# Optimization experiments

Measured on AMD Instinct MI355X. Metric: run time of the kernel, lower is better.

The kernel has to match this reference:

```python
import jax, jax.numpy as jnp
import numpy as np

D = 1024; H = 8; QLR = 384; KVLR = 256; NOPE = 128; ROPE = 64; VD = 128
E = 8; TOPK = 2; INTER = 512; NSH = 2; B = 2; T = 2048
QKD = NOPE + ROPE  # 192


def _rms(x, w, eps=1e-6):
    return x * jax.lax.rsqrt(jnp.mean(x * x, axis=-1, keepdims=True) + eps) * w


def _rope(x, cos, sin):
    # x: [B,T,h,ROPE]; pairs are consecutive elements (torch view(...,-1,2)).
    x0 = x[..., 0::2]
    x1 = x[..., 1::2]
    c = cos[None, :, None, :]
    s = sin[None, :, None, :]
    y0 = x0 * c - x1 * s
    y1 = x0 * s + x1 * c
    return jnp.stack([y0, y1], axis=-1).reshape(x.shape)


def setup_inputs() -> dict:
    key = jax.random.key(0)
    ks = jax.random.split(key, 12)
    def w(k, shape, scale=0.02):
        return jax.random.normal(k, shape, dtype=jnp.float32) * scale
    inv = 1.0 / (10000.0 ** (jnp.arange(0, ROPE, 2, dtype=jnp.float32) / ROPE))
    ang = jnp.arange(T, dtype=jnp.float32)[:, None] * inv[None, :]  # [T, ROPE//2]
    return {
        "x": jax.random.normal(ks[0], (B, T, D), dtype=jnp.float32),
        "freqs_cos": jnp.cos(ang),
        "freqs_sin": jnp.sin(ang),
        "rmsn1_w": jnp.ones((D,), jnp.float32),
        "rmsn2_w": jnp.ones((D,), jnp.float32),
        "latent_w": w(ks[1], (D, QLR + KVLR + ROPE)),
        "q_norm_w": jnp.ones((QLR,), jnp.float32),
        "q_up_w": w(ks[2], (QLR, H * QKD)),
        "kv_norm_w": jnp.ones((KVLR,), jnp.float32),
        "kv_up_w": w(ks[3], (KVLR, H * (NOPE + VD))),
        "c_proj_w": w(ks[4], (D, D)),
        "gate_w": w(ks[5], (D, E)),
        "sh_w1": w(ks[6], (D, INTER * NSH)),
        "sh_w2": w(ks[7], (INTER * NSH, D)),
        "sh_w3": w(ks[8], (D, INTER * NSH)),
        "e_w1": w(ks[9], (E, D, INTER)),
        "e_w2": w(ks[10], (E, INTER, D)),
        "e_w3": w(ks[11], (E, D, INTER)),
    }


def reference(x, freqs_cos, freqs_sin, rmsn1_w, rmsn2_w, latent_w, q_norm_w,
              q_up_w, kv_norm_w, kv_up_w, c_proj_w, gate_w, sh_w1, sh_w2,
              sh_w3, e_w1, e_w2, e_w3):
    Bx, Tx, _ = x.shape
    # ---- MLA attention ----
    h = _rms(x, rmsn1_w)
    lat = h @ latent_w
    q_l, kv_l, k_r = jnp.split(lat, [QLR, QLR + KVLR], axis=-1)
    q = (_rms(q_l, q_norm_w) @ q_up_w).reshape(Bx, Tx, H, QKD)
    q_n, q_r = q[..., :NOPE], q[..., NOPE:]
    q_r = _rope(q_r, freqs_cos, freqs_sin)
    q = jnp.concatenate([q_n, q_r], axis=-1)  # [B,T,H,QKD]
    kv = (_rms(kv_l, kv_norm_w) @ kv_up_w).reshape(Bx, Tx, H, NOPE + VD)
    k_n, v = kv[..., :NOPE], kv[..., NOPE:]
    k_r = _rope(k_r[:, :, None, :], freqs_cos, freqs_sin)
    k_r = jnp.broadcast_to(k_r, (Bx, Tx, H, ROPE))
    k = jnp.concatenate([k_n, k_r], axis=-1)
    scale = 1.0 / jnp.sqrt(jnp.float32(QKD))
    scores = jnp.einsum('bqhd,bkhd->bhqk', q, k) * scale
    causal = jnp.tril(jnp.ones((Tx, Tx), dtype=bool))
    scores = jnp.where(causal, scores, jnp.finfo(scores.dtype).min)
    attn = jax.nn.softmax(scores, axis=-1)
    y = jnp.einsum('bhqk,bkhd->bqhd', attn, v).reshape(Bx, Tx, D)
    x = x + y @ c_proj_w
    # ---- DeepSeekMoE ----
    h2 = _rms(x, rmsn2_w).reshape(-1, D)  # [N, D]
    y_sh = (jax.nn.silu(h2 @ sh_w1) * (h2 @ sh_w3)) @ sh_w2
    scores_g = jax.nn.softmax(h2 @ gate_w, axis=-1)  # [N, E]
    w_top, idx = jax.lax.top_k(scores_g, TOPK)  # weights == gathered original scores
    # combine weights per expert (route_scale = 1.0)
    cw = jnp.sum(jax.nn.one_hot(idx, E, dtype=h2.dtype) * w_top[..., None], axis=1)  # [N, E]
    h1 = jnp.einsum('nd,edi->eni', h2, e_w1)
    h3 = jnp.einsum('nd,edi->eni', h2, e_w3)
    out_e = jnp.einsum('eni,eid->end', jax.nn.silu(h1) * h3, e_w2)  # [E, N, D]
    y_moe = y_sh + jnp.einsum('end,ne->nd', out_e, cw)
    return x + y_moe.reshape(Bx, Tx, D)
```

## Files before the change

kernel.cpp:

```cpp
#include <hip/hip_runtime.h>
#include <hip/hip_bf16.h>
#include <math.h>

#define D_ 1024
#define H_ 8
#define QLR_ 384
#define KVLR_ 256
#define NOPE_ 128
#define ROPE_ 64
#define VD_ 128
#define E_ 8
#define INTER_ 512
#define B_ 2
#define T_ 2048
#define QKD_ 192
#define NTOK (B_*T_)
#define LSTR 4608
#define MAXMB 72

typedef __attribute__((ext_vector_type(8))) short short8;
typedef __attribute__((ext_vector_type(4))) float f32x4;
typedef __attribute__((ext_vector_type(4))) unsigned short us4;

__device__ __forceinline__ unsigned short f2bf(float f) {
  union { float f; unsigned u; } v; v.f = f;
  return (unsigned short)((v.u + 0x7FFFu + ((v.u >> 16) & 1u)) >> 16);
}
__device__ __forceinline__ float bf2f(unsigned short h) {
  union { unsigned u; float f; } v; v.u = ((unsigned)h) << 16;
  return v.f;
}

#define GLD16(SRC, DST) __builtin_amdgcn_global_load_lds( \
    (__attribute__((address_space(1))) void*)(SRC), \
    (__attribute__((address_space(3))) void*)(DST), 16, 0, 0)

#define DPPF(v, ctrl) __int_as_float(__builtin_amdgcn_update_dpp(0, __float_as_int(v), ctrl, 0xF, 0xF, true))
__device__ __forceinline__ float dppmax16(float v) {
  v = fmaxf(v, DPPF(v, 0xB1));
  v = fmaxf(v, DPPF(v, 0x4E));
  v = fmaxf(v, DPPF(v, 0x124));
  v = fmaxf(v, DPPF(v, 0x128));
  return v;
}
__device__ __forceinline__ float dppsum16(float v) {
  v += DPPF(v, 0xB1);
  v += DPPF(v, 0x4E);
  v += DPPF(v, 0x124);
  v += DPPF(v, 0x128);
  return v;
}

__device__ __forceinline__ void trans32(const float* __restrict__ src, unsigned short* __restrict__ dst,
                                        int R, int C, int c0, int r0, float (*tile)[33]) {
  int tx = threadIdx.x & 31, ty = threadIdx.x >> 5;
  #pragma unroll
  for (int i = 0; i < 4; ++i) {
    int rr = ty + i * 8;
    tile[rr][tx] = src[(size_t)(r0 + rr) * C + c0 + tx];
  }
  __syncthreads();
  #pragma unroll
  for (int i = 0; i < 4; ++i) {
    int rr = ty + i * 8;
    dst[(size_t)(c0 + rr) * R + r0 + tx] = f2bf(tile[tx][rr]);
  }
}
__device__ __forceinline__ void trans32p(const float* __restrict__ src, unsigned short* __restrict__ dst,
                                         int K, int C1, int c0, int r0, int f, float (*tile)[33]) {
  int tx = threadIdx.x & 31, ty = threadIdx.x >> 5;
  #pragma unroll
  for (int i = 0; i < 4; ++i) {
    int rr = ty + i * 8;
    tile[rr][tx] = src[(size_t)(r0 + rr) * C1 + c0 + tx];
  }
  __syncthreads();
  #pragma unroll
  for (int i = 0; i < 4; ++i) {
    int cc = ty + i * 8;
    int c = c0 + cc;
    int n = ((c >> 4) << 5) + (c & 15) + f;
    dst[(size_t)n * K + r0 + tx] = f2bf(tile[tx][cc]);
  }
}

__global__ __launch_bounds__(256) void prep1(
    const float* __restrict__ x, const float* __restrict__ rw, unsigned short* __restrict__ h_bf,
    const float* __restrict__ latent_w, unsigned short* __restrict__ Wlat) {
  __shared__ float tile[32][33];
  int b = blockIdx.x;
  if (b < NTOK) {
    int tid = threadIdx.x;
    const float* xr = x + (size_t)b * D_;
    float v[4]; float ss = 0.f;
    #pragma unroll
    for (int j = 0; j < 4; ++j) { v[j] = xr[tid + j * 256]; ss += v[j] * v[j]; }
    for (int o = 1; o < 64; o <<= 1) ss += __shfl_xor(ss, o);
    if ((tid & 63) == 0) tile[32][tid >> 6] = ss;
    __syncthreads();
    float inv = 1.f / sqrtf((tile[32][0] + tile[32][1] + tile[32][2] + tile[32][3]) / D_ + 1e-6f);
    #pragma unroll
    for (int j = 0; j < 4; ++j) {
      int i = tid + j * 256;
      h_bf[(size_t)b * D_ + i] = f2bf(v[j] * inv * rw[i]);
    }
    return;
  }
  b -= NTOK;
  trans32(latent_w, Wlat, 1024, 704, (b % 22) * 32, (b / 22) * 32, tile);
}

__global__ __launch_bounds__(256) void prep2(
    const unsigned short* __restrict__ h_bf, const unsigned short* __restrict__ Wlat,
    unsigned short* __restrict__ lat,
    const float* __restrict__ q_up_w, unsigned short* __restrict__ Wqup,
    const float* __restrict__ kv_up_w, unsigned short* __restrict__ Wkv,
    const float* __restrict__ c_proj_w, unsigned short* __restrict__ Wcp,
    const float* __restrict__ sh_w1, const float* __restrict__ sh_w3, unsigned short* __restrict__ Wsh13,
    const float* __restrict__ sh_w2, unsigned short* __restrict__ Wsh2,
    const float* __restrict__ e_w1, const float* __restrict__ e_w3, unsigned short* __restrict__ Wew13,
    const float* __restrict__ e_w2, unsigned short* __restrict__ Wew2) {
  __shared__ __align__(16) unsigned short As[128 * 32];
  __shared__ __align__(16) unsigned short Bs[128 * 32];
  __shared__ float tile[32][33];
  int b = blockIdx.x;
  if (b < 192) {
    const int tid = threadIdx.x, lane = tid & 63, wave = tid >> 6;
    const int wm = wave >> 1, wn = wave & 1;
    const int bm = (b / 6) * 128, bn = (b % 6) * 128;
    const int r = lane & 15, g = lane >> 4;
    f32x4 acc[4][4];
    #pragma unroll
    for (int i = 0; i < 4; ++i)
      #pragma unroll
      for (int j = 0; j < 4; ++j) acc[i][j] = (f32x4)0.f;
    const int rl0 = wave * 16 + (lane >> 2), rl1 = rl0 + 64;
    const int kc = (lane & 3) * 8;
    char* AsB = (char*)As; char* BsB = (char*)Bs;
    for (int k0 = 0; k0 < 1024; k0 += 32) {
      GLD16(h_bf + (size_t)(bm + rl0) * 1024 + k0 + kc, AsB + wave * 1024);
      GLD16(h_bf + (size_t)(bm + rl1) * 1024 + k0 + kc, AsB + (wave + 4) * 1024);
      GLD16(Wlat + (size_t)(bn + rl0) * 1024 + k0 + kc, BsB + wave * 1024);
      GLD16(Wlat + (size_t)(bn + rl1) * 1024 + k0 + kc, BsB + (wave + 4) * 1024);
      __syncthreads();
      short8 af[4], bfr[4];
      #pragma unroll
      for (int mi = 0; mi < 4; ++mi)
        af[mi] = *(const short8*)(As + (wm * 64 + mi * 16 + r) * 32 + g * 8);
      #pragma unroll
      for (int nj = 0; nj < 4; ++nj)
        bfr[nj] = *(const short8*)(Bs + (wn * 64 + nj * 16 + r) * 32 + g * 8);
      #pragma unroll
      for (int mi = 0; mi < 4; ++mi)
        #pragma unroll
        for (int nj = 0; nj < 4; ++nj)
          acc[mi][nj] = __builtin_amdgcn_mfma_f32_16x16x32_bf16(af[mi], bfr[nj], acc[mi][nj], 0, 0, 0);
      __syncthreads();
    }
    const int orow0 = wm * 64 + g * 4;
    const int ocol0 = bn + wn * 64 + r;
    #pragma unroll
    for (int mi = 0; mi < 4; ++mi)
      #pragma unroll
      for (int reg = 0; reg < 4; ++reg) {
        int mrow = bm + orow0 + mi * 16 + reg;
        size_t bas = (size_t)mrow * 768 + ocol0;
        #pragma unroll
        for (int nj = 0; nj < 4; ++nj) lat[bas + nj * 16] = f2bf(acc[mi][nj][reg]);
      }
    return;
  }
  b -= 192;
  if (b < 576) { trans32(q_up_w, Wqup, 384, 1536, (b % 48) * 32, (b / 48) * 32, tile); return; }
  b -= 576;
  if (b < 512) { trans32(kv_up_w, Wkv, 256, 2048, (b % 64) * 32, (b / 64) * 32, tile); return; }
  b -= 512;
  if (b < 1024) { trans32(c_proj_w, Wcp, 1024, 1024, (b % 32) * 32, (b / 32) * 32, tile); return; }
  b -= 1024;
  if (b < 1024) { trans32(sh_w2, Wsh2, 1024, 1024, (b % 32) * 32, (b / 32) * 32, tile); return; }
  b -= 1024;
  if (b < 2048) {
    int z = b / 1024, idx = b % 1024;
    trans32p(z ? sh_w3 : sh_w1, Wsh13, 1024, 1024, (idx % 32) * 32, (idx / 32) * 32, z * 16, tile);
    return;
  }
  b -= 2048;
  if (b < 8192) {
    int z = b / 512, idx = b % 512;
    int bat = z >> 1, f = (z & 1) * 16;
    const float* src = ((z & 1) ? e_w3 : e_w1) + (size_t)bat * 1024 * 512;
    trans32p(src, Wew13 + (size_t)bat * 1024 * 1024, 1024, 512, (idx % 16) * 32, (idx / 16) * 32, f, tile);
    return;
  }
  b -= 8192;
  {
    int z = b / 512, idx = b % 512;
    trans32(e_w2 + (size_t)z * 512 * 1024, Wew2 + (size_t)z * 1024 * 512,
            512, 1024, (idx % 32) * 32, (idx / 32) * 32, tile);
  }
}

__global__ __launch_bounds__(256) void lat_post(
    const unsigned short* __restrict__ lat, const float* __restrict__ qw,
    const float* __restrict__ kw, const float* __restrict__ fc, const float* __restrict__ fs,
    unsigned short* __restrict__ qn, unsigned short* __restrict__ kvn,
    unsigned short* __restrict__ kr) {
  int row = blockIdx.x, tid = threadIdx.x;
  int lane = tid & 63, wv = tid >> 6;
  const unsigned short* lr = lat + (size_t)row * 768;
  float s1 = 0.f, s2 = 0.f;
  for (int i = tid; i < QLR_; i += 256) { float v = bf2f(lr[i]); s1 += v * v; }
  { float v = bf2f(lr[QLR_ + tid]); s2 = v * v; }
  for (int o = 1; o < 64; o <<= 1) { s1 += __shfl_xor(s1, o); s2 += __shfl_xor(s2, o); }
  __shared__ float red[8];
  if (lane == 0) { red[wv] = s1; red[4 + wv] = s2; }
  __syncthreads();
  float inv1 = 1.f / sqrtf((red[0] + red[1] + red[2] + red[3]) / QLR_ + 1e-6f);
  float inv2 = 1.f / sqrtf((red[4] + red[5] + red[6] + red[7]) / KVLR_ + 1e-6f);
  for (int i = tid; i < QLR_; i += 256)
    qn[(size_t)row * QLR_ + i] = f2bf(bf2f(lr[i]) * inv1 * qw[i]);
  kvn[(size_t)row * KVLR_ + tid] = f2bf(bf2f(lr[QLR_ + tid]) * inv2 * kw[tid]);
  if (tid < 32) {
    int t = row & (T_ - 1);
    float c = fc[t * 32 + tid], s = fs[t * 32 + tid];
    float x0 = bf2f(lr[640 + 2 * tid]), x1 = bf2f(lr[640 + 2 * tid + 1]);
    kr[(size_t)row * ROPE_ + 2 * tid]     = f2bf(x0 * c - x1 * s);
    kr[(size_t)row * ROPE_ + 2 * tid + 1] = f2bf(x0 * s + x1 * c);
  }
}

template<int MODE>
__global__ __launch_bounds__(256) void gemm_bf16(
    const unsigned short* __restrict__ A, const unsigned short* __restrict__ Bt,
    void* __restrict__ Cv, int M, int N, int K,
    const float* __restrict__ addv) {
  __shared__ __align__(16) unsigned short As[128 * 32];
  __shared__ __align__(16) unsigned short Bs[128 * 32];
  const int tid = threadIdx.x;
  const int lane = tid & 63, wave = tid >> 6;
  const int wm = wave >> 1, wn = wave & 1;
  const int bm = blockIdx.y * 128, bn = blockIdx.x * 128;
  const int r = lane & 15, g = lane >> 4;

  f32x4 acc[4][4];
  #pragma unroll
  for (int i = 0; i < 4; ++i)
    #pragma unroll
    for (int j = 0; j < 4; ++j) acc[i][j] = (f32x4)0.f;

  const int rl0 = wave * 16 + (lane >> 2);
  const int rl1 = rl0 + 64;
  const int kc = (lane & 3) * 8;
  char* AsB = (char*)As; char* BsB = (char*)Bs;

  for (int k0 = 0; k0 < K; k0 += 32) {
    GLD16(A + (size_t)(bm + rl0) * K + k0 + kc, AsB + wave * 1024);
    GLD16(A + (size_t)(bm + rl1) * K + k0 + kc, AsB + (wave + 4) * 1024);
    GLD16(Bt + (size_t)(bn + rl0) * K + k0 + kc, BsB + wave * 1024);
    GLD16(Bt + (size_t)(bn + rl1) * K + k0 + kc, BsB + (wave + 4) * 1024);
    __syncthreads();
    short8 af[4], bfr[4];
    #pragma unroll
    for (int mi = 0; mi < 4; ++mi)
      af[mi] = *(const short8*)(As + (wm * 64 + mi * 16 + r) * 32 + g * 8);
    #pragma unroll
    for (int nj = 0; nj < 4; ++nj)
      bfr[nj] = *(const short8*)(Bs + (wn * 64 + nj * 16 + r) * 32 + g * 8);
    #pragma unroll
    for (int mi = 0; mi < 4; ++mi)
      #pragma unroll
      for (int nj = 0; nj < 4; ++nj)
        acc[mi][nj] = __builtin_amdgcn_mfma_f32_16x16x32_bf16(af[mi], bfr[nj], acc[mi][nj], 0, 0, 0);
    __syncthreads();
  }

  const int orow0 = wm * 64 + g * 4;
  const int ocol0 = bn + wn * 64 + r;
  #pragma unroll
  for (int mi = 0; mi < 4; ++mi) {
    #pragma unroll
    for (int reg = 0; reg < 4; ++reg) {
      int mrow = bm + orow0 + mi * 16 + reg;
      size_t bas = (size_t)mrow * N + ocol0;
      if (MODE == 0) {
        unsigned short* C = (unsigned short*)Cv;
        #pragma unroll
        for (int nj = 0; nj < 4; ++nj) C[bas + nj * 16] = f2bf(acc[mi][nj][reg]);
      } else {
        float* C = (float*)Cv;
        #pragma unroll
        for (int nj = 0; nj < 4; ++nj) C[bas + nj * 16] = acc[mi][nj][reg] + addv[bas + nj * 16];
      }
    }
  }
}

__global__ __launch_bounds__(256) void gemm_qkv(
    const unsigned short* __restrict__ qn, const unsigned short* __restrict__ Wqup,
    const unsigned short* __restrict__ kvn, const unsigned short* __restrict__ Wkv,
    unsigned short* __restrict__ qq, unsigned short* __restrict__ kvb,
    unsigned short* __restrict__ vtg) {
  __shared__ __align__(16) unsigned short As[128 * 32];
  __shared__ __align__(16) unsigned short Bs[128 * 32];
  const int tid = threadIdx.x;
  const int lane = tid & 63, wave = tid >> 6;
  const int wm = wave >> 1, wn = wave & 1;
  const bool isQ = blockIdx.x < 12;
  const int bx = isQ ? blockIdx.x : blockIdx.x - 12;
  const unsigned short* A  = isQ ? qn : kvn;
  const unsigned short* Bt = isQ ? Wqup : Wkv;
  const int K = isQ ? QLR_ : KVLR_;
  const int bm = blockIdx.y * 128, bn = bx * 128;
  const int r = lane & 15, g = lane >> 4;

  f32x4 acc[4][4];
  #pragma unroll
  for (int i = 0; i < 4; ++i)
    #pragma unroll
    for (int j = 0; j < 4; ++j) acc[i][j] = (f32x4)0.f;

  const int rl0 = wave * 16 + (lane >> 2);
  const int rl1 = rl0 + 64;
  const int kc = (lane & 3) * 8;
  char* AsB = (char*)As; char* BsB = (char*)Bs;

  for (int k0 = 0; k0 < K; k0 += 32) {
    GLD16(A + (size_t)(bm + rl0) * K + k0 + kc, AsB + wave * 1024);
    GLD16(A + (size_t)(bm + rl1) * K + k0 + kc, AsB + (wave + 4) * 1024);
    GLD16(Bt + (size_t)(bn + rl0) * K + k0 + kc, BsB + wave * 1024);
    GLD16(Bt + (size_t)(bn + rl1) * K + k0 + kc, BsB + (wave + 4) * 1024);
    __syncthreads();
    short8 af[4], bfr[4];
    #pragma unroll
    for (int mi = 0; mi < 4; ++mi)
      af[mi] = *(const short8*)(As + (wm * 64 + mi * 16 + r) * 32 + g * 8);
    #pragma unroll
    for (int nj = 0; nj < 4; ++nj)
      bfr[nj] = *(const short8*)(Bs + (wn * 64 + nj * 16 + r) * 32 + g * 8);
    #pragma unroll
    for (int mi = 0; mi < 4; ++mi)
      #pragma unroll
      for (int nj = 0; nj < 4; ++nj)
        acc[mi][nj] = __builtin_amdgcn_mfma_f32_16x16x32_bf16(af[mi], bfr[nj], acc[mi][nj], 0, 0, 0);
    __syncthreads();
  }

  if (isQ) {
    const int orow0 = wm * 64 + g * 4;
    const int ocol0 = bn + wn * 64 + r;
    #pragma unroll
    for (int mi = 0; mi < 4; ++mi)
      #pragma unroll
      for (int reg = 0; reg < 4; ++reg) {
        int mrow = bm + orow0 + mi * 16 + reg;
        size_t bas = (size_t)mrow * 1536 + ocol0;
        #pragma unroll
        for (int nj = 0; nj < 4; ++nj) qq[bas + nj * 16] = f2bf(acc[mi][nj][reg]);
      }
  } else {
    const int colbase = bn + wn * 64;
    const int b = bm >> 11;
    const int hh = colbase >> 8;
    if ((colbase & 255) < 128) {
      #pragma unroll
      for (int mi = 0; mi < 4; ++mi)
        #pragma unroll
        for (int reg = 0; reg < 4; ++reg) {
          int mrow = bm + wm * 64 + mi * 16 + g * 4 + reg;
          size_t bas = (size_t)mrow * 1024 + hh * 128 + (colbase & 255) + r;
          #pragma unroll
          for (int nj = 0; nj < 4; ++nj) kvb[bas + nj * 16] = f2bf(acc[mi][nj][reg]);
        }
    } else {
      const int tl0 = (bm & 2047) + wm * 64 + g * 4;
      const int d0 = (colbase & 255) - 128 + r;
      const size_t bhbase = (size_t)(b * 8 + hh) * 64;
      #pragma unroll
      for (int mi = 0; mi < 4; ++mi) {
        int t = tl0 + mi * 16;
        size_t tb = (bhbase + (t >> 5)) * 4096 + (t & 31);
        #pragma unroll
        for (int nj = 0; nj < 4; ++nj) {
          int d = d0 + nj * 16;
          us4 pk;
          #pragma unroll
          for (int reg = 0; reg < 4; ++reg) pk[reg] = f2bf(acc[mi][nj][reg]);
          *(us4*)(vtg + tb + (size_t)d * 32) = pk;
        }
      }
    }
  }
}

__global__ __launch_bounds__(256) void gemm_ffn13(
    const unsigned short* __restrict__ h2b, const unsigned short* __restrict__ Wsh13,
    unsigned short* __restrict__ t1m,
    const unsigned short* __restrict__ Wew13, unsigned short* __restrict__ ehm,
    const int* __restrict__ lists, const int* __restrict__ map, const int* __restrict__ sbase) {
  __shared__ __align__(16) unsigned short As[128 * 32];
  __shared__ __align__(16) unsigned short Bs[128 * 32];
  const int i = blockIdx.x;
  const bool isSh = i < 512;
  const int tid = threadIdx.x, lane = tid & 63, wave = tid >> 6;
  const int wm = wave >> 1, wn = wave & 1;
  const int r = lane & 15, g = lane >> 4;
  const int rl0 = wave * 16 + (lane >> 2), rl1 = rl0 + 64;
  const int kc = (lane & 3) * 8;

  int bn, e = 0, ib = 0, bm = 0;
  const unsigned short* Bt;
  int ar0, ar1;
  const unsigned short* A;
  if (isSh) {
    bn = (i & 15) * 128; bm = (i >> 4) * 128;
    Bt = Wsh13; A = h2b;
    ar0 = bm + rl0; ar1 = bm + rl1;
  } else {
    int j = i - 512;
    bn = (j & 7) * 128;
    int mb = map[j >> 3];
    if (mb < 0) return;
    e = mb >> 16; ib = mb & 0xFFFF;
    Bt = Wew13 + (size_t)e * 1024 * 1024; A = h2b;
    ar0 = lists[e * LSTR + ib * 128 + rl0]; if (ar0 < 0) ar0 = 0;
    ar1 = lists[e * LSTR + ib * 128 + rl1]; if (ar1 < 0) ar1 = 0;
  }

  f32x4 acc[4][4];
  #pragma unroll
  for (int a = 0; a < 4; ++a)
    #pragma unroll
    for (int bj = 0; bj < 4; ++bj) acc[a][bj] = (f32x4)0.f;
  char* AsB = (char*)As; char* BsB = (char*)Bs;

  for (int k0 = 0; k0 < 1024; k0 += 32) {
    GLD16(A + (size_t)ar0 * 1024 + k0 + kc, AsB + wave * 1024);
    GLD16(A + (size_t)ar1 * 1024 + k0 + kc, AsB + (wave + 4) * 1024);
    GLD16(Bt + (size_t)(bn + rl0) * 1024 + k0 + kc, BsB + wave * 1024);
    GLD16(Bt + (size_t)(bn + rl1) * 1024 + k0 + kc, BsB + (wave + 4) * 1024);
    __syncthreads();
    short8 af[4], bfr[4];
    #pragma unroll
    for (int mi = 0; mi < 4; ++mi)
      af[mi] = *(const short8*)(As + (wm * 64 + mi * 16 + r) * 32 + g * 8);
    #pragma unroll
    for (int nj = 0; nj < 4; ++nj)
      bfr[nj] = *(const short8*)(Bs + (wn * 64 + nj * 16 + r) * 32 + g * 8);
    #pragma unroll
    for (int mi = 0; mi < 4; ++mi)
      #pragma unroll
      for (int nj = 0; nj < 4; ++nj)
        acc[mi][nj] = __builtin_amdgcn_mfma_f32_16x16x32_bf16(af[mi], bfr[nj], acc[mi][nj], 0, 0, 0);
    __syncthreads();
  }

  if (isSh) {
    const int hc = ((bn + wn * 64) >> 1) + r;
    #pragma unroll
    for (int mi = 0; mi < 4; ++mi)
      #pragma unroll
      for (int reg = 0; reg < 4; ++reg) {
        int mrow = bm + wm * 64 + mi * 16 + g * 4 + reg;
        #pragma unroll
        for (int p = 0; p < 2; ++p) {
          float a = acc[mi][2 * p][reg], b3 = acc[mi][2 * p + 1][reg];
          t1m[(size_t)mrow * 1024 + hc + p * 16] = f2bf((a / (1.f + __expf(-a))) * b3);
        }
      }
  } else {
    const int sb = sbase[e] + ib * 128;
    const int hc = ((bn + wn * 64) >> 1) + r;
    #pragma unroll
    for (int mi = 0; mi < 4; ++mi)
      #pragma unroll
      for (int reg = 0; reg < 4; ++reg) {
        int srow = sb + wm * 64 + mi * 16 + g * 4 + reg;
        #pragma unroll
        for (int p = 0; p < 2; ++p) {
          float a = acc[mi][2 * p][reg], b3 = acc[mi][2 * p + 1][reg];
          ehm[(size_t)srow * 512 + hc + p * 16] = f2bf((a / (1.f + __expf(-a))) * b3);
        }
      }
  }
}

__global__ __launch_bounds__(256) void gemm_ffn2(
    const unsigned short* __restrict__ t1m, const unsigned short* __restrict__ Wsh2,
    const unsigned short* __restrict__ ehm, const unsigned short* __restrict__ Wew2,
    float* __restrict__ out,
    const int* __restrict__ lists, const int* __restrict__ map, const int* __restrict__ sbase,
    const float* __restrict__ cw) {
  __shared__ __align__(16) unsigned short As[128 * 32];
  __shared__ __align__(16) unsigned short Bs[128 * 32];
  const int i = blockIdx.x;
  const bool isSh = i < 256;
  const int tid = threadIdx.x, lane = tid & 63, wave = tid >> 6;
  const int wm = wave >> 1, wn = wave & 1;
  const int r = lane & 15, g = lane >> 4;
  const int rl0 = wave * 16 + (lane >> 2), rl1 = rl0 + 64;
  const int kc = (lane & 3) * 8;

  int bn, e = 0, ib = 0, bm = 0, K;
  const unsigned short* A;
  const unsigned short* Bt;
  if (isSh) {
    bn = (i & 7) * 128; bm = (i >> 3) * 128;
    A = t1m; Bt = Wsh2; K = 1024;
  } else {
    int j = i - 256;
    bn = (j & 7) * 128;
    int mb = map[j >> 3];
    if (mb < 0) return;
    e = mb >> 16; ib = mb & 0xFFFF;
    bm = sbase[e] + ib * 128;
    A = ehm; Bt = Wew2 + (size_t)e * 512 * 1024; K = 512;
  }

  f32x4 acc[4][4];
  #pragma unroll
  for (int a = 0; a < 4; ++a)
    #pragma unroll
    for (int bj = 0; bj < 4; ++bj) acc[a][bj] = (f32x4)0.f;
  char* AsB = (char*)As; char* BsB = (char*)Bs;

  for (int k0 = 0; k0 < K; k0 += 32) {
    GLD16(A + (size_t)(bm + rl0) * K + k0 + kc, AsB + wave * 1024);
    GLD16(A + (size_t)(bm + rl1) * K + k0 + kc, AsB + (wave + 4) * 1024);
    GLD16(Bt + (size_t)(bn + rl0) * K + k0 + kc, BsB + wave * 1024);
    GLD16(Bt + (size_t)(bn + rl1) * K + k0 + kc, BsB + (wave + 4) * 1024);
    __syncthreads();
    short8 af[4], bfr[4];
    #pragma unroll
    for (int mi = 0; mi < 4; ++mi)
      af[mi] = *(const short8*)(As + (wm * 64 + mi * 16 + r) * 32 + g * 8);
    #pragma unroll
    for (int nj = 0; nj < 4; ++nj)
      bfr[nj] = *(const short8*)(Bs + (wn * 64 + nj * 16 + r) * 32 + g * 8);
    #pragma unroll
    for (int mi = 0; mi < 4; ++mi)
      #pragma unroll
      for (int nj = 0; nj < 4; ++nj)
        acc[mi][nj] = __builtin_amdgcn_mfma_f32_16x16x32_bf16(af[mi], bfr[nj], acc[mi][nj], 0, 0, 0);
    __syncthreads();
  }

  const int ocol0 = bn + wn * 64 + r;
  if (isSh) {
    #pragma unroll
    for (int mi = 0; mi < 4; ++mi)
      #pragma unroll
      for (int reg = 0; reg < 4; ++reg) {
        int mrow = bm + wm * 64 + mi * 16 + g * 4 + reg;
        #pragma unroll
        for (int nj = 0; nj < 4; ++nj)
          atomicAdd(out + (size_t)mrow * 1024 + ocol0 + nj * 16, acc[mi][nj][reg]);
      }
  } else {
    #pragma unroll
    for (int mi = 0; mi < 4; ++mi)
      #pragma unroll
      for (int reg = 0; reg < 4; ++reg) {
        int orow = wm * 64 + mi * 16 + g * 4 + reg;
        int tok = lists[e * LSTR + ib * 128 + orow];
        if (tok >= 0) {
          float wt = cw[(size_t)tok * E_ + e];
          #pragma unroll
          for (int nj = 0; nj < 4; ++nj)
            atomicAdd(out + (size_t)tok * 1024 + ocol0 + nj * 16, acc[mi][nj][reg] * wt);
        }
      }
  }
}

#define AQ 128
#define AK 32
#define VP 40
__global__ __launch_bounds__(512) void attn_mfma(
    const unsigned short* __restrict__ q,
    const unsigned short* __restrict__ kv,
    const unsigned short* __restrict__ kr,
    const unsigned short* __restrict__ vt,
    const float* __restrict__ fcos, const float* __restrict__ fsin,
    unsigned short* __restrict__ po,
    float* __restrict__ pml) {
  __shared__ __align__(16) unsigned short Ks[AK * 192];
  __shared__ __align__(16) unsigned short Vl[128 * VP];
  __shared__ __align__(16) unsigned short Ps[8 * 16 * VP];
  const int tid = threadIdx.x, lane = tid & 63, wave = tid >> 6;
  const int r = lane & 15, g = lane >> 4;
  const int bh = blockIdx.y, b = bh >> 3, h = bh & 7;
  const int Stab[17] = {0,1,2,3,4,6,8,10,12,15,18,21,24,28,32,36,40};
  const int cid = 39 - (int)blockIdx.x;
  int qt = 0;
  #pragma unroll
  for (int t = 1; t <= 15; ++t) if (cid >= Stab[t]) qt = t;
  const int chunk = cid - Stab[qt];
  const int q0 = qt * AQ;
  const int ntl = 4 * (qt + 1);
  const int kb = chunk * 16;
  const int ke = (kb + 16 < ntl) ? kb + 16 : ntl;
  const size_t bT = (size_t)b * T_;
  const unsigned short* vbase = vt + (size_t)bh * 64 * 4096;
  char* KsB = (char*)Ks;

  short8 qf[6];
  const int qrow = q0 + wave * 16 + r;
  {
    const unsigned short* qb = q + ((bT + qrow) * H_ + h) * 192;
    #pragma unroll
    for (int kk = 0; kk < 6; ++kk) qf[kk] = *(const short8*)(qb + kk * 32 + g * 8);
    #pragma unroll
    for (int kk = 4; kk < 6; ++kk) {
      int i0 = (kk - 4) * 16 + g * 4;
      #pragma unroll
      for (int p = 0; p < 4; ++p) {
        float cc = fcos[qrow * 32 + i0 + p], sn = fsin[qrow * 32 + i0 + p];
        float x0 = bf2f((unsigned short)qf[kk][2 * p]), x1 = bf2f((unsigned short)qf[kk][2 * p + 1]);
        qf[kk][2 * p]     = (short)f2bf(x0 * cc - x1 * sn);
        qf[kk][2 * p + 1] = (short)f2bf(x0 * sn + x1 * cc);
      }
    }
  }

  float m_i[4], l_i[4];
  f32x4 o[8];
  #pragma unroll
  for (int i = 0; i < 4; ++i) { m_i[i] = -1e30f; l_i[i] = 0.f; }
  #pragma unroll
  for (int cb = 0; cb < 8; ++cb) o[cb] = (f32x4)0.f;

  const float scale2 = 0.07216878364870322f * 1.44269504088896f;

  const int kr0r = tid / 24, kr0c = tid % 24;
  const bool k1v = tid < 256;
  const int kr1r = (tid + 512) / 24, kr1c = (tid + 512) % 24;

  short8 kreg0, kreg1, vreg;
  {
    int kk0 = kb * AK;
    kreg0 = (kr0c < 16)
      ? *(const short8*)(kv + ((bT + kk0 + kr0r) * H_ + h) * 128 + kr0c * 8)
      : *(const short8*)(kr + (bT + kk0 + kr0r) * 64 + (kr0c - 16) * 8);
    if (k1v)
      kreg1 = (kr1c < 16)
        ? *(const short8*)(kv + ((bT + kk0 + kr1r) * H_ + h) * 128 + kr1c * 8)
        : *(const short8*)(kr + (bT + kk0 + kr1r) * 64 + (kr1c - 16) * 8);
    vreg = *(const short8*)(vbase + (size_t)kb * 4096 + tid * 8);
  }

  for (int kt = kb; kt < ke; ++kt) {
    __builtin_amdgcn_s_barrier();
    __builtin_amdgcn_sched_barrier(0);
    *(short8*)(KsB + ((kr0r * 384 + kr0c * 16) ^ ((kr0r & 7) << 4))) = kreg0;
    if (k1v)
      *(short8*)(KsB + ((kr1r * 384 + kr1c * 16) ^ ((kr1r & 7) << 4))) = kreg1;
    *(short8*)(Vl + (tid >> 2) * VP + (tid & 3) * 8) = vreg;
    asm volatile("s_waitcnt lgkmcnt(0)" ::: "memory");
    __builtin_amdgcn_s_barrier();
    __builtin_amdgcn_sched_barrier(0);

    if (kt + 1 < ke) {
      int k1 = (kt + 1) * AK;
      kreg0 = (kr0c < 16)
        ? *(const short8*)(kv + ((bT + k1 + kr0r) * H_ + h) * 128 + kr0c * 8)
        : *(const short8*)(kr + (bT + k1 + kr0r) * 64 + (kr0c - 16) * 8);
      if (k1v)
        kreg1 = (kr1c < 16)
          ? *(const short8*)(kv + ((bT + k1 + kr1r) * H_ + h) * 128 + kr1c * 8)
          : *(const short8*)(kr + (bT + k1 + kr1r) * 64 + (kr1c - 16) * 8);
      vreg = *(const short8*)(vbase + (size_t)(kt + 1) * 4096 + tid * 8);
    }

    const int k0 = kt * AK;
    f32x4 sf0 = (f32x4)0.f, sf1 = (f32x4)0.f;
    {
      int ksw = (r & 7) << 4;
      __builtin_amdgcn_s_setprio(1);
      #pragma unroll
      for (int kk = 0; kk < 6; ++kk) {
        short8 b0 = *(const short8*)(KsB + ((r * 384 + kk * 64 + g * 16) ^ ksw));
        short8 b1 = *(const short8*)(KsB + (((16 + r) * 384 + kk * 64 + g * 16) ^ ksw));
        sf0 = __builtin_amdgcn_mfma_f32_16x16x32_bf16(qf[kk], b0, sf0, 0, 0, 0);
        sf1 = __builtin_amdgcn_mfma_f32_16x16x32_bf16(qf[kk], b1, sf1, 0, 0, 0);
      }
      __builtin_amdgcn_s_setprio(0);
    }

    float fac[4];
    bool needs = false;
    const bool bnd = (k0 + AK > q0);
    #pragma unroll
    for (int reg = 0; reg < 4; ++reg) {
      float s0 = sf0[reg] * scale2;
      float s1 = sf1[reg] * scale2;
      if (bnd) {
        int qp = q0 + wave * 16 + g * 4 + reg;
        if (k0 + r > qp) s0 = -1e30f;
        if (k0 + 16 + r > qp) s1 = -1e30f;
      }
      float mt = dppmax16(fmaxf(s0, s1));
      float fc = 1.f, mn = m_i[reg];
      if (mt > mn + 8.f) {
        mn = mt; fc = exp2f(m_i[reg] - mn); m_i[reg] = mn; needs = true;
      }
      float e0 = exp2f(s0 - mn), e1 = exp2f(s1 - mn);
      float rs = dppsum16(e0 + e1);
      l_i[reg] = l_i[reg] * fc + rs;
      fac[reg] = fc;
      __hip_bfloat162 pk = __float22bfloat162_rn(float2{e0, e1});
      unsigned u = *(unsigned*)&pk;
      int prow = g * 4 + reg;
      Ps[wave * 16 * VP + prow * VP + r] = (unsigned short)u;
      Ps[wave * 16 * VP + prow * VP + 16 + r] = (unsigned short)(u >> 16);
    }
    if (__any(needs)) {
      #pragma unroll
      for (int cb = 0; cb < 8; ++cb)
        #pragma unroll
        for (int reg = 0; reg < 4; ++reg) o[cb][reg] *= fac[reg];
    }
    short8 pa = *(const short8*)(Ps + wave * 16 * VP + r * VP + g * 8);
    __builtin_amdgcn_s_setprio(1);
    #pragma unroll
    for (int cb = 0; cb < 8; ++cb) {
      short8 vb = *(const short8*)(Vl + (cb * 16 + r) * VP + g * 8);
      o[cb] = __builtin_amdgcn_mfma_f32_16x16x32_bf16(pa, vb, o[cb], 0, 0, 0);
    }
    __builtin_amdgcn_s_setprio(0);
  }

  const int slab = bh * 40 + cid;
  unsigned short* pob = po + (size_t)slab * 16384;
  float* pmlb = pml + (size_t)slab * 256;
  #pragma unroll
  for (int reg = 0; reg < 4; ++reg) {
    int row = wave * 16 + g * 4 + reg;
    if (r == 0) { pmlb[row * 2] = m_i[reg]; pmlb[row * 2 + 1] = l_i[reg]; }
    #pragma unroll
    for (int cb = 0; cb < 8; ++cb)
      pob[row * 128 + cb * 16 + r] = f2bf(o[cb][reg]);
  }
}

__global__ __launch_bounds__(512) void attn_combine(
    const unsigned short* __restrict__ po, const float* __restrict__ pml,
    unsigned short* __restrict__ y) {
  const int qt = blockIdx.x, bh = blockIdx.y, b = bh >> 3, h = bh & 7;
  const int Stab[17] = {0,1,2,3,4,6,8,10,12,15,18,21,24,28,32,36,40};
  const int s0 = bh * 40 + Stab[qt];
  const int nc = Stab[qt + 1] - Stab[qt];
  const int row = threadIdx.x >> 2;
  const int qp = threadIdx.x & 3;
  float mj[4], lj[4];
  float m = -1e30f;
  for (int j = 0; j < nc; ++j) {
    mj[j] = pml[(size_t)(s0 + j) * 256 + row * 2];
    lj[j] = pml[(size_t)(s0 + j) * 256 + row * 2 + 1];
    m = fmaxf(m, mj[j]);
  }
  float lsum = 0.f;
  float ej[4];
  for (int j = 0; j < nc; ++j) {
    ej[j] = exp2f(mj[j] - m);
    lsum += lj[j] * ej[j];
  }
  float inv = 1.f / lsum;
  unsigned short* yb = y + ((size_t)(b * T_ + qt * 128 + row)) * 1024 + h * 128 + qp * 32;
  #pragma unroll
  for (int v = 0; v < 4; ++v) {
    float accv[8];
    #pragma unroll
    for (int jj = 0; jj < 8; ++jj) accv[jj] = 0.f;
    for (int j = 0; j < nc; ++j) {
      const unsigned short* oj = po + (size_t)(s0 + j) * 16384 + row * 128 + qp * 32 + v * 8;
      short8 a = *(const short8*)oj;
      float w = ej[j];
      #pragma unroll
      for (int jj = 0; jj < 8; ++jj) accv[jj] += bf2f((unsigned short)a[jj]) * w;
    }
    short8 wv;
    #pragma unroll
    for (int jj = 0; jj < 8; ++jj) wv[jj] = (short)f2bf(accv[jj] * inv);
    *(short8*)(yb + v * 8) = wv;
  }
}

__global__ __launch_bounds__(256) void rms2_gate(
    const float* __restrict__ xo, const float* __restrict__ rw, const float* __restrict__ gw,
    unsigned short* __restrict__ h2b, float* __restrict__ cw) {
  int row = blockIdx.x, tid = threadIdx.x;
  int lane = tid & 63, wv = tid >> 6;
  const float* xr = xo + (size_t)row * D_;
  float v[4]; float ss = 0.f;
  #pragma unroll
  for (int j = 0; j < 4; ++j) { v[j] = xr[tid + j * 256]; ss += v[j] * v[j]; }
  for (int o = 1; o < 64; o <<= 1) ss += __shfl_xor(ss, o);
  __shared__ float red[4];
  if (lane == 0) red[wv] = ss;
  __syncthreads();
  float inv = 1.f / sqrtf((red[0] + red[1] + red[2] + red[3]) / D_ + 1e-6f);
  float a[E_] = {0, 0, 0, 0, 0, 0, 0, 0};
  #pragma unroll
  for (int j = 0; j < 4; ++j) {
    int i = tid + j * 256;
    float hv = v[j] * inv * rw[i];
    h2b[(size_t)row * D_ + i] = f2bf(hv);
    const float* wr = gw + (size_t)i * E_;
    #pragma unroll
    for (int e = 0; e < E_; ++e) a[e] += hv * wr[e];
  }
  #pragma unroll
  for (int e = 0; e < E_; ++e) {
    float t = a[e];
    for (int o = 1; o < 64; o <<= 1) t += __shfl_xor(t, o);
    a[e] = t;
  }
  __shared__ float ga[4][E_];
  if (lane == 0)
    #pragma unroll
    for (int e = 0; e < E_; ++e) ga[wv][e] = a[e];
  __syncthreads();
  if (tid == 0) {
    float lg[E_];
    #pragma unroll
    for (int e = 0; e < E_; ++e) lg[e] = ga[0][e] + ga[1][e] + ga[2][e] + ga[3][e];
    float mx = lg[0];
    #pragma unroll
    for (int e = 1; e < E_; ++e) mx = fmaxf(mx, lg[e]);
    float sum = 0.f; float p[E_];
    #pragma unroll
    for (int e = 0; e < E_; ++e) { p[e] = __expf(lg[e] - mx); sum += p[e]; }
    float is = 1.f / sum;
    int i1 = 0; float b1 = p[0];
    #pragma unroll
    for (int e = 1; e < E_; ++e) if (p[e] > b1) { b1 = p[e]; i1 = e; }
    int i2 = -1; float b2 = -1.f;
    #pragma unroll
    for (int e = 0; e < E_; ++e) if (e != i1 && p[e] > b2) { b2 = p[e]; i2 = e; }
    #pragma unroll
    for (int e = 0; e < E_; ++e)
      cw[(size_t)row * E_ + e] = (e == i1) ? b1 * is : (e == i2 ? b2 * is : 0.f);
  }
}

__global__ __launch_bounds__(256) void moe_build(const float* __restrict__ cw,
                                                 int* __restrict__ lists, int* __restrict__ counts) {
  int e = blockIdx.x, tid = threadIdx.x;
  int lane = tid & 63, wv = tid >> 6;
  __shared__ int wsum[4];
  __shared__ int base;
  if (tid == 0) base = 0;
  __syncthreads();
  for (int c0 = 0; c0 < NTOK; c0 += 256) {
    int tok = c0 + tid;
    bool f = cw[(size_t)tok * E_ + e] > 0.f;
    unsigned long long m = __ballot(f);
    int pos = __popcll(m & ((1ull << lane) - 1ull));
    if (lane == 0) wsum[wv] = __popcll(m);
    __syncthreads();
    int woff = base;
    #pragma unroll
    for (int w = 0; w < 4; ++w) if (w < wv) woff += wsum[w];
    if (f) lists[e * LSTR + woff + pos] = tok;
    __syncthreads();
    if (tid == 0) base += wsum[0] + wsum[1] + wsum[2] + wsum[3];
    __syncthreads();
  }
  int cnt = base;
  int padded = (cnt + 127) & ~127;
  for (int i2 = cnt + tid; i2 < padded; i2 += 256) lists[e * LSTR + i2] = -1;
  if (tid == 0) { counts[e] = cnt; counts[8 + e] = padded >> 7; }
}

__global__ void moe_finalize(const int* __restrict__ counts, int* __restrict__ map,
                             int* __restrict__ sbase) {
  if (threadIdx.x == 0 && blockIdx.x == 0) {
    int cum = 0;
    for (int e = 0; e < E_; ++e) {
      sbase[e] = cum * 128;
      int nb = counts[8 + e];
      for (int i = 0; i < nb; ++i) map[cum + i] = (e << 16) | i;
      cum += nb;
    }
    for (; cum < MAXMB; ++cum) map[cum] = -1;
  }
}

extern "C" void kernel_launch(void* const* d_in, const int* in_sizes, int n_in,
                              void* d_out, int out_size, void* d_ws, size_t ws_size,
                              hipStream_t stream) {
  const float* x        = (const float*)d_in[0];
  const float* fcos     = (const float*)d_in[1];
  const float* fsin     = (const float*)d_in[2];
  const float* rmsn1_w  = (const float*)d_in[3];
  const float* rmsn2_w  = (const float*)d_in[4];
  const float* latent_w = (const float*)d_in[5];
  const float* q_norm_w = (const float*)d_in[6];
  const float* q_up_w   = (const float*)d_in[7];
  const float* kv_norm_w= (const float*)d_in[8];
  const float* kv_up_w  = (const float*)d_in[9];
  const float* c_proj_w = (const float*)d_in[10];
  const float* gate_w   = (const float*)d_in[11];
  const float* sh_w1    = (const float*)d_in[12];
  const float* sh_w2    = (const float*)d_in[13];
  const float* sh_w3    = (const float*)d_in[14];
  const float* e_w1     = (const float*)d_in[15];
  const float* e_w2     = (const float*)d_in[16];
  const float* e_w3     = (const float*)d_in[17];
  float* out = (float*)d_out;

  char* base = (char*)d_ws;
  size_t off = 0;
  auto take = [&](size_t bytes) { char* p = base + off; off += (bytes + 255) & ~(size_t)255; return p; };
  unsigned short* Wlat  = (unsigned short*)take((size_t)768 * 1024 * 2);
  unsigned short* Wqup  = (unsigned short*)take((size_t)1536 * 384 * 2);
  unsigned short* Wkv   = (unsigned short*)take((size_t)2048 * 256 * 2);
  unsigned short* Wcp   = (unsigned short*)take((size_t)1024 * 1024 * 2);
  unsigned short* Wsh13 = (unsigned short*)take((size_t)2048 * 1024 * 2);
  unsigned short* Wsh2  = (unsigned short*)take((size_t)1024 * 1024 * 2);
  unsigned short* Wew13 = (unsigned short*)take((size_t)8 * 1024 * 1024 * 2);
  unsigned short* Wew2  = (unsigned short*)take((size_t)8 * 1024 * 512 * 2);
  float* cw             = (float*)take((size_t)NTOK * E_ * 4);
  int* lists            = (int*)take((size_t)E_ * LSTR * 4);
  int* counts           = (int*)take(64 * 4);
  int* map              = (int*)take(MAXMB * 4);
  int* sbase            = (int*)take(E_ * 4);
  unsigned short* Vtg   = (unsigned short*)take((size_t)16 * 64 * 4096 * 2);
  unsigned short* kr    = (unsigned short*)take((size_t)NTOK * 64 * 2);

  size_t actStart = off;
  size_t aoff = actStart;
  auto takeA = [&](size_t bytes) { char* p = base + aoff; aoff += (bytes + 255) & ~(size_t)255; return p; };
  unsigned short* h_bf = (unsigned short*)takeA((size_t)NTOK * 1024 * 2);
  unsigned short* lat  = (unsigned short*)takeA((size_t)NTOK * 768 * 2);
  unsigned short* qn   = (unsigned short*)takeA((size_t)NTOK * 384 * 2);
  unsigned short* kvn  = (unsigned short*)takeA((size_t)NTOK * 256 * 2);
  unsigned short* qq   = (unsigned short*)takeA((size_t)NTOK * 1536 * 2);
  unsigned short* kvb  = (unsigned short*)takeA((size_t)NTOK * 1024 * 2);
  unsigned short* y    = (unsigned short*)takeA((size_t)NTOK * 1024 * 2);
  unsigned short* po   = (unsigned short*)takeA((size_t)640 * 16384 * 2);
  float* pml           = (float*)takeA((size_t)640 * 256 * 4);

  size_t coff = actStart;
  auto takeC = [&](size_t bytes) { char* p = base + coff; coff += (bytes + 255) & ~(size_t)255; return p; };
  unsigned short* h2b  = (unsigned short*)takeC((size_t)NTOK * 1024 * 2);
  unsigned short* t1m  = (unsigned short*)takeC((size_t)NTOK * 1024 * 2);
  unsigned short* ehm  = (unsigned short*)takeC((size_t)9216 * 512 * 2);

  dim3 blk(256);

  prep1<<<dim3(NTOK + 704), blk, 0, stream>>>(x, rmsn1_w, h_bf, latent_w, Wlat);
  prep2<<<dim3(192 + 576 + 512 + 1024 + 1024 + 2048 + 8192 + 4096), blk, 0, stream>>>(
      h_bf, Wlat, lat, q_up_w, Wqup, kv_up_w, Wkv, c_proj_w, Wcp,
      sh_w1, sh_w3, Wsh13, sh_w2, Wsh2, e_w1, e_w3, Wew13, e_w2, Wew2);
  lat_post<<<NTOK, blk, 0, stream>>>(lat, q_norm_w, kv_norm_w, fcos, fsin, qn, kvn, kr);
  gemm_qkv<<<dim3(28, 32), blk, 0, stream>>>(qn, Wqup, kvn, Wkv, qq, kvb, Vtg);
  attn_mfma<<<dim3(40, 16), dim3(512), 0, stream>>>(qq, kvb, kr, Vtg, fcos, fsin, po, pml);
  attn_combine<<<dim3(16, 16), dim3(512), 0, stream>>>(po, pml, y);
  gemm_bf16<1><<<dim3(8, 32), blk, 0, stream>>>(y, Wcp, out, NTOK, 1024, 1024, x);
  rms2_gate<<<NTOK, blk, 0, stream>>>(out, rmsn2_w, gate_w, h2b, cw);
  moe_build<<<E_, blk, 0, stream>>>(cw, lists, counts);
  moe_finalize<<<1, 64, 0, stream>>>(counts, map, sbase);
  gemm_ffn13<<<dim3(1088), blk, 0, stream>>>(h2b, Wsh13, t1m, Wew13, ehm, lists, map, sbase);
  gemm_ffn2<<<dim3(832), blk, 0, stream>>>(t1m, Wsh2, ehm, Wew2, out, lists, map, sbase, cw);
}
```

Before: 344.9 us.

## Split attention KV range into finer chunks and fold MoE finalize into build

The attention split-K now uses chunks of 8 key tiles instead of 16, raising the chunk count per head from 40 to 72. This gives more blocks and better load balance across CUs for the causal attention. The combine kernel is unrolled to handle up to 8 partials per query tile. Separately, the single-thread moe_finalize launch is removed: the last moe_build block, found with an atomic counter that rms2_gate resets, builds the block map. The costs are more partial-output traffic and combine work, plus reliance on atomic ordering.

```diff
diff --git a/kernel.cpp b/kernel.cpp
--- a/kernel.cpp
+++ b/kernel.cpp
@@ -17,6 +17,7 @@
 #define NTOK (B_*T_)
 #define LSTR 4608
 #define MAXMB 72
+#define NCH 72
 
 typedef __attribute__((ext_vector_type(8))) short short8;
 typedef __attribute__((ext_vector_type(4))) float f32x4;
@@ -589,16 +590,16 @@
   const int tid = threadIdx.x, lane = tid & 63, wave = tid >> 6;
   const int r = lane & 15, g = lane >> 4;
   const int bh = blockIdx.y, b = bh >> 3, h = bh & 7;
-  const int Stab[17] = {0,1,2,3,4,6,8,10,12,15,18,21,24,28,32,36,40};
-  const int cid = 39 - (int)blockIdx.x;
+  const int Stab[17] = {0,1,2,4,6,9,12,16,20,25,30,36,42,49,56,64,72};
+  const int cid = (NCH - 1) - (int)blockIdx.x;
   int qt = 0;
   #pragma unroll
   for (int t = 1; t <= 15; ++t) if (cid >= Stab[t]) qt = t;
   const int chunk = cid - Stab[qt];
   const int q0 = qt * AQ;
   const int ntl = 4 * (qt + 1);
-  const int kb = chunk * 16;
-  const int ke = (kb + 16 < ntl) ? kb + 16 : ntl;
+  const int kb = chunk * 8;
+  const int ke = (kb + 8 < ntl) ? kb + 8 : ntl;
   const size_t bT = (size_t)b * T_;
   const unsigned short* vbase = vt + (size_t)bh * 64 * 4096;
   char* KsB = (char*)Ks;
@@ -729,7 +730,7 @@
     __builtin_amdgcn_s_setprio(0);
   }
 
-  const int slab = bh * 40 + cid;
+  const int slab = bh * NCH + cid;
   unsigned short* pob = po + (size_t)slab * 16384;
   float* pmlb = pml + (size_t)slab * 256;
   #pragma unroll
@@ -746,23 +747,28 @@
     const unsigned short* __restrict__ po, const float* __restrict__ pml,
     unsigned short* __restrict__ y) {
   const int qt = blockIdx.x, bh = blockIdx.y, b = bh >> 3, h = bh & 7;
-  const int Stab[17] = {0,1,2,3,4,6,8,10,12,15,18,21,24,28,32,36,40};
-  const int s0 = bh * 40 + Stab[qt];
+  const int Stab[17] = {0,1,2,4,6,9,12,16,20,25,30,36,42,49,56,64,72};
+  const int s0 = bh * NCH + Stab[qt];
   const int nc = Stab[qt + 1] - Stab[qt];
   const int row = threadIdx.x >> 2;
   const int qp = threadIdx.x & 3;
-  float mj[4], lj[4];
+  float mj[8], lj[8], ej[8];
   float m = -1e30f;
-  for (int j = 0; j < nc; ++j) {
-    mj[j] = pml[(size_t)(s0 + j) * 256 + row * 2];
-    lj[j] = pml[(size_t)(s0 + j) * 256 + row * 2 + 1];
-    m = fmaxf(m, mj[j]);
+  #pragma unroll
+  for (int j = 0; j < 8; ++j) {
+    if (j < nc) {
+      mj[j] = pml[(size_t)(s0 + j) * 256 + row * 2];
+      lj[j] = pml[(size_t)(s0 + j) * 256 + row * 2 + 1];
+      m = fmaxf(m, mj[j]);
+    }
   }
   float lsum = 0.f;
-  float ej[4];
-  for (int j = 0; j < nc; ++j) {
-    ej[j] = exp2f(mj[j] - m);
-    lsum += lj[j] * ej[j];
+  #pragma unroll
+  for (int j = 0; j < 8; ++j) {
+    if (j < nc) {
+      ej[j] = exp2f(mj[j] - m);
+      lsum += lj[j] * ej[j];
+    }
   }
   float inv = 1.f / lsum;
   unsigned short* yb = y + ((size_t)(b * T_ + qt * 128 + row)) * 1024 + h * 128 + qp * 32;
@@ -771,12 +777,15 @@
     float accv[8];
     #pragma unroll
     for (int jj = 0; jj < 8; ++jj) accv[jj] = 0.f;
-    for (int j = 0; j < nc; ++j) {
-      const unsigned short* oj = po + (size_t)(s0 + j) * 16384 + row * 128 + qp * 32 + v * 8;
-      short8 a = *(const short8*)oj;
-      float w = ej[j];
-      #pragma unroll
-      for (int jj = 0; jj < 8; ++jj) accv[jj] += bf2f((unsigned short)a[jj]) * w;
+    #pragma unroll
+    for (int j = 0; j < 8; ++j) {
+      if (j < nc) {
+        const unsigned short* oj = po + (size_t)(s0 + j) * 16384 + row * 128 + qp * 32 + v * 8;
+        short8 a = *(const short8*)oj;
+        float w = ej[j];
+        #pragma unroll
+        for (int jj = 0; jj < 8; ++jj) accv[jj] += bf2f((unsigned short)a[jj]) * w;
+      }
     }
     short8 wv;
     #pragma unroll
@@ -787,9 +796,10 @@
 
 __global__ __launch_bounds__(256) void rms2_gate(
     const float* __restrict__ xo, const float* __restrict__ rw, const float* __restrict__ gw,
-    unsigned short* __restrict__ h2b, float* __restrict__ cw) {
+    unsigned short* __restrict__ h2b, float* __restrict__ cw, int* __restrict__ done) {
   int row = blockIdx.x, tid = threadIdx.x;
   int lane = tid & 63, wv = tid >> 6;
+  if (row == 0 && tid == 0) *done = 0;
   const float* xr = xo + (size_t)row * D_;
   float v[4]; float ss = 0.f;
   #pragma unroll
@@ -844,7 +854,9 @@
 }
 
 __global__ __launch_bounds__(256) void moe_build(const float* __restrict__ cw,
-                                                 int* __restrict__ lists, int* __restrict__ counts) {
+                                                 int* __restrict__ lists, int* __restrict__ counts,
+                                                 int* __restrict__ map, int* __restrict__ sbase,
+                                                 int* __restrict__ done) {
   int e = blockIdx.x, tid = threadIdx.x;
   int lane = tid & 63, wv = tid >> 6;
   __shared__ int wsum[4];
@@ -869,20 +881,21 @@
   int cnt = base;
   int padded = (cnt + 127) & ~127;
   for (int i2 = cnt + tid; i2 < padded; i2 += 256) lists[e * LSTR + i2] = -1;
-  if (tid == 0) { counts[e] = cnt; counts[8 + e] = padded >> 7; }
-}
-
-__global__ void moe_finalize(const int* __restrict__ counts, int* __restrict__ map,
-                             int* __restrict__ sbase) {
-  if (threadIdx.x == 0 && blockIdx.x == 0) {
-    int cum = 0;
-    for (int e = 0; e < E_; ++e) {
-      sbase[e] = cum * 128;
-      int nb = counts[8 + e];
-      for (int i = 0; i < nb; ++i) map[cum + i] = (e << 16) | i;
-      cum += nb;
-    }
-    for (; cum < MAXMB; ++cum) map[cum] = -1;
+  if (tid == 0) {
+    counts[e] = cnt;
+    counts[8 + e] = padded >> 7;
+    __threadfence();
+    int old = atomicAdd(done, 1);
+    if (old == E_ - 1) {
+      int cum = 0;
+      for (int ee = 0; ee < E_; ++ee) {
+        sbase[ee] = cum * 128;
+        int nb = counts[8 + ee];
+        for (int i = 0; i < nb; ++i) map[cum + i] = (ee << 16) | i;
+        cum += nb;
+      }
+      for (; cum < MAXMB; ++cum) map[cum] = -1;
+    }
   }
 }
 
@@ -925,6 +938,7 @@
   int* counts           = (int*)take(64 * 4);
   int* map              = (int*)take(MAXMB * 4);
   int* sbase            = (int*)take(E_ * 4);
+  int* done             = (int*)take(64 * 4);
   unsigned short* Vtg   = (unsigned short*)take((size_t)16 * 64 * 4096 * 2);
   unsigned short* kr    = (unsigned short*)take((size_t)NTOK * 64 * 2);
 
@@ -938,8 +952,8 @@
   unsigned short* qq   = (unsigned short*)takeA((size_t)NTOK * 1536 * 2);
   unsigned short* kvb  = (unsigned short*)takeA((size_t)NTOK * 1024 * 2);
   unsigned short* y    = (unsigned short*)takeA((size_t)NTOK * 1024 * 2);
-  unsigned short* po   = (unsigned short*)takeA((size_t)640 * 16384 * 2);
-  float* pml           = (float*)takeA((size_t)640 * 256 * 4);
+  unsigned short* po   = (unsigned short*)takeA((size_t)16 * NCH * 16384 * 2);
+  float* pml           = (float*)takeA((size_t)16 * NCH * 256 * 4);
 
   size_t coff = actStart;
   auto takeC = [&](size_t bytes) { char* p = base + coff; coff += (bytes + 255) & ~(size_t)255; return p; };
@@ -955,12 +969,11 @@
       sh_w1, sh_w3, Wsh13, sh_w2, Wsh2, e_w1, e_w3, Wew13, e_w2, Wew2);
   lat_post<<<NTOK, blk, 0, stream>>>(lat, q_norm_w, kv_norm_w, fcos, fsin, qn, kvn, kr);
   gemm_qkv<<<dim3(28, 32), blk, 0, stream>>>(qn, Wqup, kvn, Wkv, qq, kvb, Vtg);
-  attn_mfma<<<dim3(40, 16), dim3(512), 0, stream>>>(qq, kvb, kr, Vtg, fcos, fsin, po, pml);
+  attn_mfma<<<dim3(NCH, 16), dim3(512), 0, stream>>>(qq, kvb, kr, Vtg, fcos, fsin, po, pml);
   attn_combine<<<dim3(16, 16), dim3(512), 0, stream>>>(po, pml, y);
   gemm_bf16<1><<<dim3(8, 32), blk, 0, stream>>>(y, Wcp, out, NTOK, 1024, 1024, x);
-  rms2_gate<<<NTOK, blk, 0, stream>>>(out, rmsn2_w, gate_w, h2b, cw);
-  moe_build<<<E_, blk, 0, stream>>>(cw, lists, counts);
-  moe_finalize<<<1, 64, 0, stream>>>(counts, map, sbase);
+  rms2_gate<<<NTOK, blk, 0, stream>>>(out, rmsn2_w, gate_w, h2b, cw, done);
+  moe_build<<<E_, blk, 0, stream>>>(cw, lists, counts, map, sbase, done);
   gemm_ffn13<<<dim3(1088), blk, 0, stream>>>(h2b, Wsh13, t1m, Wew13, ehm, lists, map, sbase);
   gemm_ffn2<<<dim3(832), blk, 0, stream>>>(t1m, Wsh2, ehm, Wew2, out, lists, map, sbase, cw);
 }
```

Result: slower. 357.1 us (+3.5%).
